# Kernel tuning notes

Measured on AMD Instinct MI355X. Metric: run time of the kernel, lower is better.

The kernel has to match this reference:

```python
import jax, jax.numpy as jnp
import numpy as np
import math

B, S, HID = 1, 4096, 2048
H, KVH, D = 32, 8, 64
N_REP = H // KVH  # 4


def _rope(x, cos, sin):
    # x: [B, h, S, D]; cos/sin: [S, D//2]
    x2 = x.reshape(*x.shape[:-1], D // 2, 2)
    x0, x1 = x2[..., 0], x2[..., 1]
    c = cos[None, None, :, :]
    s = sin[None, None, :, :]
    # complex multiply (x0 + i x1) * (c + i s)
    o0 = x0 * c - x1 * s
    o1 = x0 * s + x1 * c
    return jnp.stack([o0, o1], axis=-1).reshape(x.shape)


def setup_inputs() -> dict:
    key = jax.random.key(0)
    ks = jax.random.split(key, 6)
    hidden_states = jax.random.normal(ks[0], (B, S, 2 * HID), dtype=jnp.float32)
    scale = 0.02
    wq = jax.random.normal(ks[1], (H * D, 2 * HID), dtype=jnp.float32) * scale
    wk = jax.random.normal(ks[2], (KVH * D, 2 * HID), dtype=jnp.float32) * scale
    wv = jax.random.normal(ks[3], (KVH * D, 2 * HID), dtype=jnp.float32) * scale
    wo = jax.random.normal(ks[4], (HID, H * D), dtype=jnp.float32) * scale
    # standard RoPE frequencies (theta=10000), shape [S, D//2]
    inv_freq = 1.0 / (10000.0 ** (np.arange(0, D, 2, dtype=np.float32) / D))
    angles = np.arange(S, dtype=np.float32)[:, None] * inv_freq[None, :]
    freqs_cos = jnp.asarray(np.cos(angles), dtype=jnp.float32)
    freqs_sin = jnp.asarray(np.sin(angles), dtype=jnp.float32)
    return {"hidden_states": hidden_states, "wq": wq, "wk": wk, "wv": wv,
            "wo": wo, "freqs_cos": freqs_cos, "freqs_sin": freqs_sin}


def reference(hidden_states, wq, wk, wv, wo, freqs_cos, freqs_sin):
    bsz, q_len, _ = hidden_states.shape
    q = (hidden_states @ wq.T).reshape(bsz, q_len, H, D).transpose(0, 2, 1, 3)   # [B,H,S,D]
    k = (hidden_states @ wk.T).reshape(bsz, q_len, KVH, D).transpose(0, 2, 1, 3)  # [B,KVH,S,D]
    v = (hidden_states @ wv.T).reshape(bsz, q_len, KVH, D).transpose(0, 2, 1, 3)
    q = _rope(q, freqs_cos, freqs_sin)
    k = _rope(k, freqs_cos, freqs_sin)
    # GQA repeat_kv
    k = jnp.repeat(k, N_REP, axis=1)  # [B,H,S,D]
    v = jnp.repeat(v, N_REP, axis=1)
    scores = jnp.einsum('bhqd,bhkd->bhqk', q, k) / math.sqrt(D)  # [B,H,S,S]
    weights = jax.nn.softmax(scores.astype(jnp.float32), axis=-1).astype(q.dtype)
    attn = jnp.einsum('bhqk,bhkd->bhqd', weights, v)  # [B,H,S,D]
    attn = attn.transpose(0, 2, 1, 3).reshape(bsz, q_len, H * D)
    return attn @ wo.T  # [B,S,HID]
```

## Files before the change

kernel.cpp:

```cpp
#include <hip/hip_runtime.h>
#include <hip/hip_bf16.h>

typedef __attribute__((ext_vector_type(4))) float f32x4;
typedef __attribute__((ext_vector_type(8))) __bf16 bf16x8;
typedef __attribute__((ext_vector_type(8))) short short8;
typedef __attribute__((ext_vector_type(4))) short short4v;
typedef __attribute__((ext_vector_type(2))) unsigned int uint2v;
typedef __attribute__((ext_vector_type(4))) unsigned int uint4v;

#define SEQ 4096
#define NQKV 3072

static __device__ __forceinline__ unsigned short f2bf(float x) {
  unsigned int u = __float_as_uint(x);
  u += 0x7fffu + ((u >> 16) & 1u);
  return (unsigned short)(u >> 16);
}
static __device__ __forceinline__ float bf2f(unsigned short b) {
  return __uint_as_float(((unsigned int)b) << 16);
}
static __device__ __forceinline__ unsigned int cvtpk_bf16(float lo, float hi) {
  unsigned int r;
  asm("v_cvt_pk_bf16_f32 %0, %1, %2" : "=v"(r) : "v"(lo), "v"(hi));
  return r;
}
static __device__ __forceinline__ float exp2_fast(float x) {
  float r;
  asm("v_exp_f32 %0, %1" : "=v"(r) : "v"(x));
  return r;
}

__global__ void cvt_all(const float* __restrict__ hs, const float* __restrict__ wq,
                        const float* __restrict__ wk, const float* __restrict__ wv,
                        const float* __restrict__ wo,
                        unsigned short* __restrict__ Xb, unsigned short* __restrict__ Wqkv,
                        unsigned short* __restrict__ Wob) {
  int i = blockIdx.x * blockDim.x + threadIdx.x;
  const float* src;
  unsigned short* dst;
  int off;
  if (i < 4194304)      { src = hs; dst = Xb;              off = i; }
  else if (i < 6291456) { src = wq; dst = Wqkv;            off = i - 4194304; }
  else if (i < 6815744) { src = wk; dst = Wqkv + 8388608;  off = i - 6291456; }
  else if (i < 7340032) { src = wv; dst = Wqkv + 10485760; off = i - 6815744; }
  else                  { src = wo; dst = Wob;             off = i - 7340032; }
  f32x4 v = ((const f32x4*)src)[off];
  short4v o;
#pragma unroll
  for (int j = 0; j < 4; ++j) o[j] = (short)f2bf(v[j]);
  ((short4v*)dst)[off] = o;
}

template <int BN, bool OUT_F32>
__global__ __launch_bounds__(512, 1) void gemm256(const unsigned short* __restrict__ A,
                                                  const unsigned short* __restrict__ Bt,
                                                  void* __restrict__ Cp,
                                                  int M, int N, int K) {
  constexpr int NJ = BN / 64;
  constexpr int TC = 16 + BN / 16;
  constexpr int SPW = (TC + 7) / 8;
  constexpr int DUP = 8 * SPW - TC;

  __shared__ unsigned short AbL[3][8192];
  __shared__ unsigned short BbL[3][BN * 32];

  const int t512 = threadIdx.x;
  const int l = t512 & 63;
  const int wid = t512 >> 6;
  const int wm = wid >> 2, wn = wid & 3;
  const int lr = l & 15, lg = l >> 4;

  const int bid = blockIdx.y * 16 + blockIdx.x;
  const int nid = (bid & 7) * 32 + (bid >> 3);
  const int m0 = (nid >> 4) * 256, n0 = (nid & 15) * BN;

  const int lrow = l >> 2;
  const int scb = ((l & 3) << 4) ^ ((lrow & 3) << 4);
  const int rswz = (lr & 3) << 4;

  f32x4 acc[8][NJ];
#pragma unroll
  for (int i = 0; i < 8; ++i)
#pragma unroll
    for (int j = 0; j < NJ; ++j) acc[i][j] = (f32x4){0.f, 0.f, 0.f, 0.f};

  auto stage = [&](int buf, int t) {
    const int kt = t * 32;
#pragma unroll
    for (int s = 0; s < SPW; ++s) {
      int id = wid * SPW + s;
      if (DUP > 0 && id >= TC) id -= DUP;
      if (id < 16) {
        const char* src = (const char*)(A + (size_t)(m0 + id * 16 + lrow) * K + kt) + scb;
        __builtin_amdgcn_global_load_lds(
            (const __attribute__((address_space(1))) void*)src,
            (__attribute__((address_space(3))) void*)&AbL[buf][id * 512], 16, 0, 0);
      } else {
        const int b = id - 16;
        const char* src = (const char*)(Bt + (size_t)(n0 + b * 16 + lrow) * K + kt) + scb;
        __builtin_amdgcn_global_load_lds(
            (const __attribute__((address_space(1))) void*)src,
            (__attribute__((address_space(3))) void*)&BbL[buf][b * 512], 16, 0, 0);
      }
    }
  };

  const int NT = K / 32;

  stage(0, 0);
  stage(1, 1);
  if constexpr (SPW == 4) asm volatile("s_waitcnt vmcnt(4)" ::: "memory");
  else                    asm volatile("s_waitcnt vmcnt(3)" ::: "memory");
  __builtin_amdgcn_s_barrier();
  asm volatile("" ::: "memory");

  int cur = 0;
  for (int t = 0; t < NT; ++t) {
    int pf = cur + 2; if (pf >= 3) pf -= 3;
    if (t + 2 < NT) stage(pf, t + 2);

    const char* Ab0 = (const char*)&AbL[cur][0] + (size_t)(wm * 128 + lr) * 64;
    const char* Bb0 = (const char*)&BbL[cur][0] + (size_t)(wn * (BN / 4) + lr) * 64;
    bf16x8 af[8], bfv[NJ];
#pragma unroll
    for (int i = 0; i < 8; ++i)
      af[i] = *(const bf16x8*)(Ab0 + i * 1024 + ((lg * 16) ^ rswz));
#pragma unroll
    for (int j = 0; j < NJ; ++j)
      bfv[j] = *(const bf16x8*)(Bb0 + j * 1024 + ((lg * 16) ^ rswz));

    __builtin_amdgcn_s_setprio(1);
#pragma unroll
    for (int i = 0; i < 8; ++i)
#pragma unroll
      for (int j = 0; j < NJ; ++j)
        acc[i][j] = __builtin_amdgcn_mfma_f32_16x16x32_bf16(af[i], bfv[j], acc[i][j], 0, 0, 0);
    __builtin_amdgcn_s_setprio(0);

    if (t + 2 < NT) {
      if constexpr (SPW == 4) asm volatile("s_waitcnt vmcnt(4)" ::: "memory");
      else                    asm volatile("s_waitcnt vmcnt(3)" ::: "memory");
    } else if (t + 1 < NT) {
      asm volatile("s_waitcnt vmcnt(0)" ::: "memory");
    }
    if (t + 1 < NT) {
      asm volatile("s_waitcnt lgkmcnt(0)" ::: "memory");
      __builtin_amdgcn_s_barrier();
      asm volatile("" ::: "memory");
    }
    cur = (cur == 2) ? 0 : cur + 1;
  }

  const int row0 = m0 + wm * 128, col0 = n0 + wn * (BN / 4);
#pragma unroll
  for (int i = 0; i < 8; ++i) {
#pragma unroll
    for (int j = 0; j < NJ; ++j) {
      const int col = col0 + j * 16 + lr;
#pragma unroll
      for (int r = 0; r < 4; ++r) {
        const int row = row0 + i * 16 + lg * 4 + r;
        if (OUT_F32)
          ((float*)Cp)[(size_t)row * N + col] = acc[i][j][r];
        else
          ((unsigned short*)Cp)[(size_t)row * N + col] = f2bf(acc[i][j][r]);
      }
    }
  }
}

__global__ void rope_scale(unsigned short* __restrict__ qkv,
                           const float* __restrict__ fc,
                           const float* __restrict__ fs) {
  int idx = blockIdx.x * blockDim.x + threadIdx.x;
  int s = idx / 1280;
  int p = idx - s * 1280;
  bool isQ = (p < 1024);
  int col = isQ ? (p * 2) : (2048 + (p - 1024) * 2);
  int fi = (col >> 1) & 31;
  float c = fc[s * 32 + fi];
  float sn = fs[s * 32 + fi];
  unsigned short* ptr = qkv + (size_t)s * NQKV + col;
  float x0 = bf2f(ptr[0]);
  float x1 = bf2f(ptr[1]);
  float o0 = x0 * c - x1 * sn;
  float o1 = x0 * sn + x1 * c;
  float scl = isQ ? 0.1803368801111204f : 1.0f;
  ptr[0] = f2bf(o0 * scl);
  ptr[1] = f2bf(o1 * scl);
}

__global__ void v_transpose(const unsigned short* __restrict__ qkv,
                            unsigned short* __restrict__ Vt) {
  __shared__ unsigned short tile[64][72];
  const int kvh = blockIdx.x;
  const int st = blockIdx.y * 64;
  const int t = threadIdx.x;
  const int sl = t >> 2, d0 = (t & 3) * 16;
  const unsigned short* src = qkv + (size_t)(st + sl) * NQKV + 2560 + kvh * 64 + d0;
  *(bf16x8*)&tile[sl][d0] = *(const bf16x8*)src;
  *(bf16x8*)&tile[sl][d0 + 8] = *(const bf16x8*)(src + 8);
  __syncthreads();
  const int dl = t >> 2, s0 = (t & 3) * 16;
  unsigned short* dst = Vt + ((size_t)kvh * 64 + dl) * 4096 + st + s0;
#pragma unroll
  for (int j2 = 0; j2 < 2; ++j2) {
    short8 v;
#pragma unroll
    for (int j = 0; j < 8; ++j) {
      const int pos = s0 + j2 * 8 + j;
      const int key = (pos & 32) + ((pos & 4) << 2) + (((pos >> 3) & 3) << 2) + (pos & 3);
      v[j] = (short)tile[key][dl];
    }
    *(short8*)(dst + j2 * 8) = v;
  }
}

__global__ __launch_bounds__(256, 4) void attn_fwd(const unsigned short* __restrict__ qkv,
                                                   const unsigned short* __restrict__ Vt,
                                                   unsigned short* __restrict__ attn) {
  __shared__ unsigned short Ks[2][4096];
  __shared__ unsigned short Vs[2][4096];

  const int t = threadIdx.x;
  const int l = t & 63;
  const int w = t >> 6;
  const int lr = l & 15, lg = l >> 4;
  const int h = blockIdx.x;
  const int kvh = h >> 2;
  const int qbase = blockIdx.y * 128 + w * 32;

  const int chunk0 = w * 2;
  const int srow = l >> 3;
  const int scol = (l & 7) * 16;
  const int sorig = scol ^ ((srow & 7) << 4);
  const char* ksrc0 = (const char*)(qkv + 2048 + kvh * 64) +
                      (size_t)(chunk0 * 8 + srow) * (NQKV * 2) + sorig;
  const char* ksrc1 = ksrc0 + 8 * (NQKV * 2);
  const char* vsrc0 = (const char*)(Vt + (size_t)kvh * 64 * 4096) +
                      (size_t)(chunk0 * 8 + srow) * 8192 + sorig;
  const char* vsrc1 = vsrc0 + 8 * 8192;

  const int x = (lr & 7) << 4;
  const int x6 = x & 64, x45 = x & 48;
  const int offA = lr * 128 + x6 + ((lg * 16) ^ x45);
  const int offB = lr * 128 + (64 ^ x6) + ((lg * 16) ^ x45);

  bf16x8 qf[2][2];
#pragma unroll
  for (int qi = 0; qi < 2; ++qi) {
    const unsigned short* qr = qkv + (size_t)(qbase + qi * 16 + lr) * NQKV + h * 64;
    qf[qi][0] = *(const bf16x8*)(qr + lg * 8);
    qf[qi][1] = *(const bf16x8*)(qr + 32 + lg * 8);
  }

  f32x4 ls4[2];
  f32x4 o[2][4];
#pragma unroll
  for (int qi = 0; qi < 2; ++qi) {
    ls4[qi] = (f32x4){0.f, 0.f, 0.f, 0.f};
#pragma unroll
    for (int c4 = 0; c4 < 4; ++c4) o[qi][c4] = (f32x4){0.f, 0.f, 0.f, 0.f};
  }

  auto stage = [&](int buf, int tile) {
    const size_t kadv = (size_t)tile * 64 * (NQKV * 2);
    const size_t vadv = (size_t)tile * 128;
    __builtin_amdgcn_global_load_lds(
        (const __attribute__((address_space(1))) void*)(ksrc0 + kadv),
        (__attribute__((address_space(3))) void*)&Ks[buf][chunk0 * 512], 16, 0, 0);
    __builtin_amdgcn_global_load_lds(
        (const __attribute__((address_space(1))) void*)(ksrc1 + kadv),
        (__attribute__((address_space(3))) void*)&Ks[buf][(chunk0 + 1) * 512], 16, 0, 0);
    __builtin_amdgcn_global_load_lds(
        (const __attribute__((address_space(1))) void*)(vsrc0 + vadv),
        (__attribute__((address_space(3))) void*)&Vs[buf][chunk0 * 512], 16, 0, 0);
    __builtin_amdgcn_global_load_lds(
        (const __attribute__((address_space(1))) void*)(vsrc1 + vadv),
        (__attribute__((address_space(3))) void*)&Vs[buf][(chunk0 + 1) * 512], 16, 0, 0);
  };

  stage(0, 0);
  asm volatile("s_waitcnt vmcnt(0)" ::: "memory");
  __syncthreads();

  const int NT = SEQ / 64;
  for (int tt = 0; tt < NT; ++tt) {
    const int buf = tt & 1;
    if (tt + 1 < NT) stage(buf ^ 1, tt + 1);

    const char* Ksb = (const char*)Ks[buf];
    const char* Vsb = (const char*)Vs[buf];

    f32x4 sc[2][4];
    __builtin_amdgcn_s_setprio(1);
#pragma unroll
    for (int sI = 0; sI < 4; ++sI) {
      bf16x8 kf0 = *(const bf16x8*)(Ksb + offA + sI * 2048);
      bf16x8 kf1 = *(const bf16x8*)(Ksb + offB + sI * 2048);
#pragma unroll
      for (int qi = 0; qi < 2; ++qi) {
        f32x4 c = (f32x4){0.f, 0.f, 0.f, 0.f};
        c = __builtin_amdgcn_mfma_f32_16x16x32_bf16(kf0, qf[qi][0], c, 0, 0, 0);
        c = __builtin_amdgcn_mfma_f32_16x16x32_bf16(kf1, qf[qi][1], c, 0, 0, 0);
        sc[qi][sI] = c;
      }
    }
    __builtin_amdgcn_s_setprio(0);

    bf16x8 pa[2][2];
#pragma unroll
    for (int qi = 0; qi < 2; ++qi) {
      float p[4][4];
#pragma unroll
      for (int sI = 0; sI < 4; ++sI)
#pragma unroll
        for (int r = 0; r < 4; ++r) p[sI][r] = exp2_fast(sc[qi][sI][r]);
#pragma unroll
      for (int sI = 0; sI < 4; ++sI)
#pragma unroll
        for (int r = 0; r < 4; ++r) ls4[qi][r] += p[sI][r];
      uint4v u1, u2;
      u1[0] = cvtpk_bf16(p[0][0], p[0][1]); u1[1] = cvtpk_bf16(p[0][2], p[0][3]);
      u1[2] = cvtpk_bf16(p[1][0], p[1][1]); u1[3] = cvtpk_bf16(p[1][2], p[1][3]);
      u2[0] = cvtpk_bf16(p[2][0], p[2][1]); u2[1] = cvtpk_bf16(p[2][2], p[2][3]);
      u2[2] = cvtpk_bf16(p[3][0], p[3][1]); u2[3] = cvtpk_bf16(p[3][2], p[3][3]);
      pa[qi][0] = __builtin_bit_cast(bf16x8, u1);
      pa[qi][1] = __builtin_bit_cast(bf16x8, u2);
    }

    __builtin_amdgcn_s_setprio(1);
#pragma unroll
    for (int c4 = 0; c4 < 4; ++c4) {
      bf16x8 v0 = *(const bf16x8*)(Vsb + offA + c4 * 2048);
      bf16x8 v1 = *(const bf16x8*)(Vsb + offB + c4 * 2048);
#pragma unroll
      for (int qi = 0; qi < 2; ++qi) {
        o[qi][c4] = __builtin_amdgcn_mfma_f32_16x16x32_bf16(pa[qi][0], v0, o[qi][c4], 0, 0, 0);
        o[qi][c4] = __builtin_amdgcn_mfma_f32_16x16x32_bf16(pa[qi][1], v1, o[qi][c4], 0, 0, 0);
      }
    }
    __builtin_amdgcn_s_setprio(0);

    if (tt + 1 < NT) {
      asm volatile("s_waitcnt vmcnt(0)" ::: "memory");
      __syncthreads();
    }
  }

#pragma unroll
  for (int qi = 0; qi < 2; ++qi) {
    float lsum = ls4[qi][0] + ls4[qi][1] + ls4[qi][2] + ls4[qi][3];
    lsum += __shfl_xor(lsum, 16, 64);
    lsum += __shfl_xor(lsum, 32, 64);
    float inv = 1.f / lsum;
    float invO[4];
#pragma unroll
    for (int r = 0; r < 4; ++r) invO[r] = __shfl(inv, 4 * lg + r, 64);
#pragma unroll
    for (int c4 = 0; c4 < 4; ++c4)
#pragma unroll
      for (int r = 0; r < 4; ++r) {
        attn[(size_t)(qbase + qi * 16 + 4 * lg + r) * 2048 + h * 64 + c4 * 16 + lr] =
            f2bf(o[qi][c4][r] * invO[r]);
      }
  }
}

extern "C" void kernel_launch(void* const* d_in, const int* in_sizes, int n_in,
                              void* d_out, int out_size, void* d_ws, size_t ws_size,
                              hipStream_t stream) {
  const float* hs = (const float*)d_in[0];
  const float* wq = (const float*)d_in[1];
  const float* wk = (const float*)d_in[2];
  const float* wv = (const float*)d_in[3];
  const float* wo = (const float*)d_in[4];
  const float* fc = (const float*)d_in[5];
  const float* fs = (const float*)d_in[6];
  float* out = (float*)d_out;

  char* ws = (char*)d_ws;
  unsigned short* Xb    = (unsigned short*)(ws);
  unsigned short* Wqkv  = (unsigned short*)(ws + (size_t)(32 << 20));
  unsigned short* Wob   = (unsigned short*)(ws + (size_t)(56 << 20));
  unsigned short* QKV   = (unsigned short*)(ws + (size_t)(64 << 20));
  unsigned short* attnb = Xb;
  unsigned short* Vtb   = (unsigned short*)(ws + (size_t)(16 << 20));

  cvt_all<<<32768, 256, 0, stream>>>(hs, wq, wk, wv, wo, Xb, Wqkv, Wob);

  gemm256<192, false><<<dim3(16, 16), 512, 0, stream>>>(Xb, Wqkv, QKV, 4096, 3072, 4096);

  v_transpose<<<dim3(8, 64), 256, 0, stream>>>(QKV, Vtb);
  rope_scale<<<20480, 256, 0, stream>>>(QKV, fc, fs);

  attn_fwd<<<dim3(32, 32), 256, 0, stream>>>(QKV, Vtb, attnb);

  gemm256<128, true><<<dim3(16, 16), 512, 0, stream>>>(attnb, Wob, out, 4096, 2048, 2048);
}
```

Before: 341.9 us.

## Split GEMM k-step into two phases interleaving LDS reads, prefetch and MFMA

Each k-iteration of the bf16 GEMM now runs in two halves. Each half loads half of the A fragments from LDS, issues half of the global-to-LDS prefetch for stage t+2, then runs half of the MFMAs, with extra barriers and sched_barriers between the halves. This is a ping-pong style schedule meant to overlap memory issue with matrix math and to reduce register pressure from holding all A fragments. The cost is two more workgroup barriers per iteration, which could add synchronization stalls.

```diff
diff --git a/kernel.cpp b/kernel.cpp
--- a/kernel.cpp
+++ b/kernel.cpp
@@ -60,6 +60,7 @@
   constexpr int TC = 16 + BN / 16;
   constexpr int SPW = (TC + 7) / 8;
   constexpr int DUP = 8 * SPW - TC;
+  constexpr int SHALF = SPW / 2;
 
   __shared__ unsigned short AbL[3][8192];
   __shared__ unsigned short BbL[3][BN * 32];
@@ -84,10 +85,10 @@
 #pragma unroll
     for (int j = 0; j < NJ; ++j) acc[i][j] = (f32x4){0.f, 0.f, 0.f, 0.f};
 
-  auto stage = [&](int buf, int t) {
-    const int kt = t * 32;
-#pragma unroll
-    for (int s = 0; s < SPW; ++s) {
+  auto stage_part = [&](int buf, int t, int s0, int s1) {
+#pragma unroll
+    for (int s = s0; s < s1; ++s) {
+      const int kt = t * 32;
       int id = wid * SPW + s;
       if (DUP > 0 && id >= TC) id -= DUP;
       if (id < 16) {
@@ -107,8 +108,8 @@
 
   const int NT = K / 32;
 
-  stage(0, 0);
-  stage(1, 1);
+  stage_part(0, 0, 0, SPW);
+  stage_part(1, 1, 0, SPW);
   if constexpr (SPW == 4) asm volatile("s_waitcnt vmcnt(4)" ::: "memory");
   else                    asm volatile("s_waitcnt vmcnt(3)" ::: "memory");
   __builtin_amdgcn_s_barrier();
@@ -117,34 +118,54 @@
   int cur = 0;
   for (int t = 0; t < NT; ++t) {
     int pf = cur + 2; if (pf >= 3) pf -= 3;
-    if (t + 2 < NT) stage(pf, t + 2);
+    const bool do_stage = (t + 2 < NT);
 
     const char* Ab0 = (const char*)&AbL[cur][0] + (size_t)(wm * 128 + lr) * 64;
     const char* Bb0 = (const char*)&BbL[cur][0] + (size_t)(wn * (BN / 4) + lr) * 64;
-    bf16x8 af[8], bfv[NJ];
-#pragma unroll
-    for (int i = 0; i < 8; ++i)
-      af[i] = *(const bf16x8*)(Ab0 + i * 1024 + ((lg * 16) ^ rswz));
+
+    bf16x8 bfv[NJ], afA[4];
 #pragma unroll
     for (int j = 0; j < NJ; ++j)
       bfv[j] = *(const bf16x8*)(Bb0 + j * 1024 + ((lg * 16) ^ rswz));
-
+#pragma unroll
+    for (int i = 0; i < 4; ++i)
+      afA[i] = *(const bf16x8*)(Ab0 + i * 1024 + ((lg * 16) ^ rswz));
+    if (do_stage) stage_part(pf, t + 2, 0, SHALF);
+    __builtin_amdgcn_s_barrier();
+    asm volatile("s_waitcnt lgkmcnt(0)" ::: "memory");
+    __builtin_amdgcn_sched_barrier(0);
     __builtin_amdgcn_s_setprio(1);
 #pragma unroll
-    for (int i = 0; i < 8; ++i)
+    for (int i = 0; i < 4; ++i)
 #pragma unroll
       for (int j = 0; j < NJ; ++j)
-        acc[i][j] = __builtin_amdgcn_mfma_f32_16x16x32_bf16(af[i], bfv[j], acc[i][j], 0, 0, 0);
+        acc[i][j] = __builtin_amdgcn_mfma_f32_16x16x32_bf16(afA[i], bfv[j], acc[i][j], 0, 0, 0);
     __builtin_amdgcn_s_setprio(0);
-
-    if (t + 2 < NT) {
+    __builtin_amdgcn_s_barrier();
+
+    bf16x8 afB[4];
+#pragma unroll
+    for (int i = 0; i < 4; ++i)
+      afB[i] = *(const bf16x8*)(Ab0 + (4 + i) * 1024 + ((lg * 16) ^ rswz));
+    if (do_stage) stage_part(pf, t + 2, SHALF, SPW);
+    __builtin_amdgcn_s_barrier();
+    asm volatile("s_waitcnt lgkmcnt(0)" ::: "memory");
+    __builtin_amdgcn_sched_barrier(0);
+    __builtin_amdgcn_s_setprio(1);
+#pragma unroll
+    for (int i = 0; i < 4; ++i)
+#pragma unroll
+      for (int j = 0; j < NJ; ++j)
+        acc[4 + i][j] = __builtin_amdgcn_mfma_f32_16x16x32_bf16(afB[i], bfv[j], acc[4 + i][j], 0, 0, 0);
+    __builtin_amdgcn_s_setprio(0);
+
+    if (do_stage) {
       if constexpr (SPW == 4) asm volatile("s_waitcnt vmcnt(4)" ::: "memory");
       else                    asm volatile("s_waitcnt vmcnt(3)" ::: "memory");
     } else if (t + 1 < NT) {
       asm volatile("s_waitcnt vmcnt(0)" ::: "memory");
     }
     if (t + 1 < NT) {
-      asm volatile("s_waitcnt lgkmcnt(0)" ::: "memory");
       __builtin_amdgcn_s_barrier();
       asm volatile("" ::: "memory");
     }
```

After: 349.4 us. 1.02x slower.
